# Performance work log

Hardware: AMD Instinct MI355X
Metric: run time of the kernel (lower is better)

## Reference

```python
import jax, jax.numpy as jnp
import numpy as np

SIGMA = 7.0
KERNEL_SIZE = int(2 * np.ceil(SIGMA * 2) + 1)  # 29
PAD = (KERNEL_SIZE - 1) // 2  # 14


def _gaussian_kernel2d():
    variance = SIGMA ** 2
    coords = jnp.arange(KERNEL_SIZE, dtype=jnp.float32)
    mean = (KERNEL_SIZE - 1) / 2.0
    xg, yg = jnp.meshgrid(coords, coords, indexing='xy')
    k = jnp.exp(-((xg - mean) ** 2 + (yg - mean) ** 2) / (2.0 * variance))
    k = k / (2.0 * np.pi * variance)
    return k / k.sum()  # [K, K]


def setup_inputs() -> dict:
    key = jax.random.key(0)
    x = jax.random.normal(key, (8, 64, 256, 256), dtype=jnp.float32)
    return {"x": x}


def reference(x):
    channels = x.shape[1]
    k2d = _gaussian_kernel2d().astype(x.dtype)
    # depthwise weights: [C, 1, K, K] (OIHW with feature_group_count=C)
    w = jnp.broadcast_to(k2d, (channels, 1, KERNEL_SIZE, KERNEL_SIZE))
    xp = jnp.pad(x, ((0, 0), (0, 0), (PAD, PAD), (PAD, PAD)), mode='reflect')
    out = jax.lax.conv_general_dilated(
        xp, w,
        window_strides=(1, 1),
        padding='VALID',
        dimension_numbers=('NCHW', 'OIHW', 'NCHW'),
        feature_group_count=channels,
    )
    return out
```

## Files before the change

### kernel.cpp

```cpp
#include <hip/hip_runtime.h>

#define IMG   256
#define TILEY 64
#define KS    29
#define PAD   14
#define LDSS  284

static constexpr float GK[15] = {
    1.0f,        0.98984780f, 0.96000544f, 0.91225408f, 0.84936581f,
    0.77483743f, 0.69256933f, 0.60653066f, 0.52045012f, 0.43756474f,
    0.36044779f, 0.29092381f, 0.23006630f, 0.17826398f, 0.13533528f
};
static constexpr float GSUM =
    GK[0] + 2.0f * (GK[1] + GK[2] + GK[3] + GK[4] + GK[5] + GK[6] + GK[7] +
                    GK[8] + GK[9] + GK[10] + GK[11] + GK[12] + GK[13] + GK[14]);
static constexpr float WT[29] = {
    GK[14]/GSUM, GK[13]/GSUM, GK[12]/GSUM, GK[11]/GSUM, GK[10]/GSUM, GK[9]/GSUM, GK[8]/GSUM,
    GK[7]/GSUM,  GK[6]/GSUM,  GK[5]/GSUM,  GK[4]/GSUM,  GK[3]/GSUM,  GK[2]/GSUM, GK[1]/GSUM,
    GK[0]/GSUM,
    GK[1]/GSUM,  GK[2]/GSUM,  GK[3]/GSUM,  GK[4]/GSUM,  GK[5]/GSUM,  GK[6]/GSUM, GK[7]/GSUM,
    GK[8]/GSUM,  GK[9]/GSUM,  GK[10]/GSUM, GK[11]/GSUM, GK[12]/GSUM, GK[13]/GSUM, GK[14]/GSUM
};

__device__ __forceinline__ int refl(int p) {
    int a = p < 0 ? -p : p;
    int b = 2 * (IMG - 1) - a;
    return a < b ? a : b;
}

__global__ __launch_bounds__(1024, 8)
void gauss_strip(const float* __restrict__ x, float* __restrict__ out) {
    __shared__ alignas(16) float s[TILEY * LDSS];

    const int t   = threadIdx.x;
    const int img = blockIdx.y;
    const int y0  = blockIdx.x * TILEY;

    const float* __restrict__ src = x   + (size_t)img * (IMG * IMG);
    float*       __restrict__ dst = out + (size_t)img * (IMG * IMG);

    {
        const int col  = t & 255;
        const int rg   = t >> 8;
        const int r0   = rg * 16;
        const int brow = y0 + r0 - PAD;

        float acc[16];
        #pragma unroll
        for (int j = 0; j < 16; ++j) acc[j] = 0.f;

        if (brow >= 0 && brow + 43 <= IMG - 1) {
            const float* p = src + (size_t)brow * IMG + col;
            #pragma unroll
            for (int sidx = 0; sidx < 16 + KS - 1; ++sidx) {
                const float v = p[sidx * IMG];
                #pragma unroll
                for (int j = 0; j < 16; ++j) {
                    const int k = sidx - j;
                    if (k >= 0 && k < KS) acc[j] += WT[k] * v;
                }
            }
        } else {
            #pragma unroll
            for (int sidx = 0; sidx < 16 + KS - 1; ++sidx) {
                const float v = src[refl(brow + sidx) * IMG + col];
                #pragma unroll
                for (int j = 0; j < 16; ++j) {
                    const int k = sidx - j;
                    if (k >= 0 && k < KS) acc[j] += WT[k] * v;
                }
            }
        }

        const int pos = PAD + col;
        #pragma unroll
        for (int j = 0; j < 16; ++j)
            s[(r0 + j) * LDSS + pos] = acc[j];
        if (col >= 1 && col <= PAD) {
            #pragma unroll
            for (int j = 0; j < 16; ++j)
                s[(r0 + j) * LDSS + (PAD - col)] = acc[j];
        } else if (col >= IMG - 1 - PAD && col <= IMG - 2) {
            #pragma unroll
            for (int j = 0; j < 16; ++j)
                s[(r0 + j) * LDSS + (2 * (IMG - 1) + PAD - col)] = acc[j];
        }
    }
    __syncthreads();

    {
        const int row = t & 63;
        const int cg  = t >> 6;
        const int c0  = cg * 16;

        float acc[16];
        #pragma unroll
        for (int c = 0; c < 16; ++c) acc[c] = 0.f;

        const float4* srow = (const float4*)&s[row * LDSS + c0];
        #pragma unroll
        for (int m = 0; m < 11; ++m) {
            const float4 v4 = srow[m];
            #pragma unroll
            for (int q = 0; q < 4; ++q) {
                const int p = 4 * m + q;
                const float v = q == 0 ? v4.x : q == 1 ? v4.y : q == 2 ? v4.z : v4.w;
                #pragma unroll
                for (int c = 0; c < 16; ++c) {
                    const int k = p - c;
                    if (k >= 0 && k < KS) acc[c] += WT[k] * v;
                }
            }
        }

        float4* orow = (float4*)&dst[(size_t)(y0 + row) * IMG + c0];
        #pragma unroll
        for (int m = 0; m < 4; ++m)
            orow[m] = make_float4(acc[4*m+0], acc[4*m+1], acc[4*m+2], acc[4*m+3]);
    }
}

extern "C" void kernel_launch(void* const* d_in, const int* in_sizes, int n_in,
                              void* d_out, int out_size, void* d_ws, size_t ws_size,
                              hipStream_t stream) {
    const float* x = (const float*)d_in[0];
    float* out = (float*)d_out;
    const int images = in_sizes[0] / (IMG * IMG);
    dim3 grid(IMG / TILEY, images);
    gauss_strip<<<grid, dim3(1024), 0, stream>>>(x, out);
}
```

Measured before the change: 80.94 us.

## Shrink row strips to 32 and vectorize vertical pass with float4 loads

Block tile height drops from 64 to 32 rows with 512 threads per block. The vertical pass now has each thread load float4 columns and produce 4 output rows instead of 16 rows of one column. This widens global loads and raises block count and occupancy. In exchange, the halo overhead grows: each thread reads 32 input rows to produce 4 outputs versus 43 for 16, so redundant global and L2 traffic increases.

Result: slower. 84.00 us (+3.8%).

```diff
diff --git a/kernel.cpp b/kernel.cpp
--- a/kernel.cpp
+++ b/kernel.cpp
@@ -1,7 +1,7 @@
 #include <hip/hip_runtime.h>
 
 #define IMG   256
-#define TILEY 64
+#define ROWS  32
 #define KS    29
 #define PAD   14
 #define LDSS  284
@@ -28,69 +28,91 @@
     return a < b ? a : b;
 }
 
-__global__ __launch_bounds__(1024, 8)
-void gauss_strip(const float* __restrict__ x, float* __restrict__ out) {
-    __shared__ alignas(16) float s[TILEY * LDSS];
+__global__ __launch_bounds__(512, 8)
+void gauss_v4(const float* __restrict__ x, float* __restrict__ out) {
+    __shared__ float s[ROWS * LDSS];
 
     const int t   = threadIdx.x;
     const int img = blockIdx.y;
-    const int y0  = blockIdx.x * TILEY;
+    const int y0  = blockIdx.x * ROWS;
 
     const float* __restrict__ src = x   + (size_t)img * (IMG * IMG);
     float*       __restrict__ dst = out + (size_t)img * (IMG * IMG);
 
     {
-        const int col  = t & 255;
-        const int rg   = t >> 8;
-        const int r0   = rg * 16;
-        const int brow = y0 + r0 - PAD;
+        const int cq   = t & 63;
+        const int rg   = t >> 6;
+        const int c0   = cq * 4;
+        const int brow = y0 + rg * 4 - PAD;
 
-        float acc[16];
+        float4 acc[4];
         #pragma unroll
-        for (int j = 0; j < 16; ++j) acc[j] = 0.f;
+        for (int j = 0; j < 4; ++j) acc[j] = make_float4(0.f, 0.f, 0.f, 0.f);
 
-        if (brow >= 0 && brow + 43 <= IMG - 1) {
-            const float* p = src + (size_t)brow * IMG + col;
+        if (brow >= 0 && brow + 31 < IMG) {
+            const float* p = src + (size_t)brow * IMG + c0;
             #pragma unroll
-            for (int sidx = 0; sidx < 16 + KS - 1; ++sidx) {
-                const float v = p[sidx * IMG];
+            for (int sdx = 0; sdx < 32; ++sdx) {
+                const float4 v = *(const float4*)(p + sdx * IMG);
                 #pragma unroll
-                for (int j = 0; j < 16; ++j) {
-                    const int k = sidx - j;
-                    if (k >= 0 && k < KS) acc[j] += WT[k] * v;
+                for (int j = 0; j < 4; ++j) {
+                    const int k = sdx - j;
+                    if (k >= 0 && k < KS) {
+                        acc[j].x += WT[k] * v.x;
+                        acc[j].y += WT[k] * v.y;
+                        acc[j].z += WT[k] * v.z;
+                        acc[j].w += WT[k] * v.w;
+                    }
                 }
             }
         } else {
             #pragma unroll
-            for (int sidx = 0; sidx < 16 + KS - 1; ++sidx) {
-                const float v = src[refl(brow + sidx) * IMG + col];
+            for (int sdx = 0; sdx < 32; ++sdx) {
+                const float4 v = *(const float4*)(src + (size_t)refl(brow + sdx) * IMG + c0);
                 #pragma unroll
-                for (int j = 0; j < 16; ++j) {
-                    const int k = sidx - j;
-                    if (k >= 0 && k < KS) acc[j] += WT[k] * v;
+                for (int j = 0; j < 4; ++j) {
+                    const int k = sdx - j;
+                    if (k >= 0 && k < KS) {
+                        acc[j].x += WT[k] * v.x;
+                        acc[j].y += WT[k] * v.y;
+                        acc[j].z += WT[k] * v.z;
+                        acc[j].w += WT[k] * v.w;
+                    }
                 }
             }
         }
 
-        const int pos = PAD + col;
         #pragma unroll
-        for (int j = 0; j < 16; ++j)
-            s[(r0 + j) * LDSS + pos] = acc[j];
-        if (col >= 1 && col <= PAD) {
+        for (int j = 0; j < 4; ++j) {
+            float* row = &s[(rg * 4 + j) * LDSS + PAD + c0];
+            *(float2*)(row)     = make_float2(acc[j].x, acc[j].y);
+            *(float2*)(row + 2) = make_float2(acc[j].z, acc[j].w);
+        }
+        if (c0 <= PAD || c0 >= IMG - 1 - PAD - 3) {
             #pragma unroll
-            for (int j = 0; j < 16; ++j)
-                s[(r0 + j) * LDSS + (PAD - col)] = acc[j];
-        } else if (col >= IMG - 1 - PAD && col <= IMG - 2) {
-            #pragma unroll
-            for (int j = 0; j < 16; ++j)
-                s[(r0 + j) * LDSS + (2 * (IMG - 1) + PAD - col)] = acc[j];
+            for (int q = 0; q < 4; ++q) {
+                const int c = c0 + q;
+                if (c >= 1 && c <= PAD) {
+                    #pragma unroll
+                    for (int j = 0; j < 4; ++j) {
+                        const float v = q == 0 ? acc[j].x : q == 1 ? acc[j].y : q == 2 ? acc[j].z : acc[j].w;
+                        s[(rg * 4 + j) * LDSS + (PAD - c)] = v;
+                    }
+                } else if (c >= IMG - 1 - PAD && c <= IMG - 2) {
+                    #pragma unroll
+                    for (int j = 0; j < 4; ++j) {
+                        const float v = q == 0 ? acc[j].x : q == 1 ? acc[j].y : q == 2 ? acc[j].z : acc[j].w;
+                        s[(rg * 4 + j) * LDSS + (2 * (IMG - 1) + PAD - c)] = v;
+                    }
+                }
+            }
         }
     }
     __syncthreads();
 
     {
-        const int row = t & 63;
-        const int cg  = t >> 6;
+        const int row = t & 31;
+        const int cg  = t >> 5;
         const int c0  = cg * 16;
 
         float acc[16];
@@ -126,6 +148,6 @@
     const float* x = (const float*)d_in[0];
     float* out = (float*)d_out;
     const int images = in_sizes[0] / (IMG * IMG);
-    dim3 grid(IMG / TILEY, images);
-    gauss_strip<<<grid, dim3(1024), 0, stream>>>(x, out);
+    dim3 grid(IMG / ROWS, images);
+    gauss_v4<<<grid, dim3(512), 0, stream>>>(x, out);
 }
```
